# Optimization experiments

Hardware: AMD Instinct MI355X
Metric: run time of the kernel (lower is better)

The kernel has to match this reference:

```python
import jax, jax.numpy as jnp
import numpy as np

B, D, E, H, L = 32768, 512, 10, 128, 2  # batch, input_dim, max_charts, expert hidden, latent_dim
RH1, RH2 = 256, 128                      # router hidden sizes
TAU = 3.0


def setup_inputs() -> dict:
    key = jax.random.key(0)
    ks = jax.random.split(key, 16)
    rnd = lambda k, *s: (jax.random.normal(k, s, jnp.float32) * 0.05)
    return {
        "x": jax.random.normal(ks[0], (B, D), jnp.float32),
        "u": jax.random.uniform(ks[1], (B, E), jnp.float32),
        # router params (last layer init ~ N(0, 0.01), bias 0, as in _init_router)
        "rw1": rnd(ks[2], D, RH1), "rb1": jnp.zeros((RH1,), jnp.float32),
        "rw2": rnd(ks[3], RH1, RH2), "rb2": jnp.zeros((RH2,), jnp.float32),
        "rw3": jax.random.normal(ks[4], (RH2, E), jnp.float32) * 0.01,
        "rb3": jnp.zeros((E,), jnp.float32),
        # stacked expert params: all 10 experts batched along leading dim
        "ew1": rnd(ks[5], E, D, H), "eb1": rnd(ks[6], E, H),
        "ew2": rnd(ks[7], E, H, H), "eb2": rnd(ks[8], E, H),
        "ew3": rnd(ks[9], E, H, L), "eb3": rnd(ks[10], E, L),
    }


def reference(x, u, rw1, rb1, rw2, rb2, rw3, rb3, ew1, eb1, ew2, eb2, ew3, eb3):
    # router MLP: D -> 256 -> 128 -> E
    h = jax.nn.relu(x @ rw1 + rb1)
    h = jax.nn.relu(h @ rw2 + rb2)
    logits = h @ rw3 + rb3                                  # [B, E]
    # gumbel_softmax(tau=3.0, hard=False): softmax((logits + gumbel)/tau)
    g = -jnp.log(-jnp.log(jnp.clip(u, 1e-10, 1.0)) + 1e-10)
    weights = jax.nn.softmax((logits + g) / TAU, axis=1)    # [B, E]
    # all 10 experts as batched GEMMs (fuses the python loop over charts)
    h1 = jax.nn.relu(jnp.einsum('bi,eio->beo', x, ew1) + eb1[None])   # [B, E, H]
    h2 = jax.nn.relu(jnp.einsum('beh,eho->beo', h1, ew2) + eb2[None]) # [B, E, H]
    zc = jnp.einsum('beh,ehl->bel', h2, ew3) + eb3[None]              # [B, E, L]
    z = jnp.einsum('be,bel->bl', weights, zc)                         # [B, L]
    chart_outputs = jnp.transpose(zc, (1, 0, 2))                      # [E, B, L]
    return z, weights, chart_outputs
```

## Files before the change

kernel.cpp:

```cpp
#include <hip/hip_runtime.h>
#include <stdint.h>

typedef __bf16 bf16x8 __attribute__((ext_vector_type(8)));
typedef float floatx4 __attribute__((ext_vector_type(4)));
typedef unsigned short ushort_t;

__device__ __forceinline__ ushort_t bf16rne(float f) {
    union { float f; unsigned u; } v; v.f = f;
    return (ushort_t)((v.u + 0x7fffu + ((v.u >> 16) & 1u)) >> 16);
}

__device__ __forceinline__ void gl_lds16(const ushort_t* g, ushort_t* l) {
    __builtin_amdgcn_global_load_lds(
        (const __attribute__((address_space(1))) unsigned int*)g,
        (__attribute__((address_space(3))) unsigned int*)l, 16, 0, 0);
}


__global__ void prep(const float* __restrict__ x, ushort_t* __restrict__ x16,
                     const float* __restrict__ ew1, ushort_t* __restrict__ ew1t,
                     const float* __restrict__ ew2, ushort_t* __restrict__ ew2t,
                     const float* __restrict__ rw1, ushort_t* __restrict__ rw1t,
                     const float* __restrict__ rw2, ushort_t* __restrict__ rw2t) {
    __shared__ ushort_t sT[64 * 65];
    int b = blockIdx.x, tid = threadIdx.x;
    if (b < 16384) {
        int i = b * 256 + tid;
        float4 f = ((const float4*)x)[i];
        union { ushort_t s[4]; uint2 v; } pk;
        pk.s[0] = bf16rne(f.x); pk.s[1] = bf16rne(f.y);
        pk.s[2] = bf16rne(f.z); pk.s[3] = bf16rne(f.w);
        ((uint2*)x16)[i] = pk.v;
        return;
    }
    const float* in; ushort_t* outp; int K, N, k0, n0;
    int i = b - 16384;
    if (i < 160) {
        int e = i >> 4, t = i & 15;
        in = ew1 + e * 65536; outp = ew1t + e * 65536;
        K = 512; N = 128; k0 = (t >> 1) * 64; n0 = (t & 1) * 64;
    } else if (i < 200) {
        i -= 160; int e = i >> 2, t = i & 3;
        in = ew2 + e * 16384; outp = ew2t + e * 16384;
        K = 128; N = 128; k0 = (t >> 1) * 64; n0 = (t & 1) * 64;
    } else if (i < 232) {
        i -= 200; in = rw1; outp = rw1t;
        K = 512; N = 256; k0 = (i >> 2) * 64; n0 = (i & 3) * 64;
    } else {
        i -= 232; in = rw2; outp = rw2t;
        K = 256; N = 128; k0 = (i >> 1) * 64; n0 = (i & 1) * 64;
    }
    {
        int c = tid & 63, r0 = tid >> 6;
#pragma unroll
        for (int p = 0; p < 16; ++p) {
            int r = r0 * 16 + p;
            sT[c * 65 + r] = bf16rne(in[(size_t)(k0 + r) * N + n0 + c]);
        }
        __syncthreads();
        int rr = tid & 63, c0 = tid >> 6;
#pragma unroll
        for (int p = 0; p < 16; ++p) {
            int cc = c0 * 16 + p;
            outp[(size_t)(n0 + cc) * K + k0 + rr] = sT[cc * 65 + rr];
        }
    }
}

__global__ __launch_bounds__(256, 3)
void fused_main(const ushort_t* __restrict__ x16,
                const ushort_t* __restrict__ rw1t, const float* __restrict__ rb1,
                const ushort_t* __restrict__ rw2t, const float* __restrict__ rb2,
                const float* __restrict__ rw3, const float* __restrict__ rb3,
                const float* __restrict__ u,
                const ushort_t* __restrict__ ew1t, const ushort_t* __restrict__ ew2t,
                const float* __restrict__ eb1, const float* __restrict__ eb2,
                const float* __restrict__ ew3, const float* __restrict__ eb3,
                float* __restrict__ wts, float* __restrict__ chart) {
    __shared__ alignas(16) ushort_t sXW[8192];
    __shared__ alignas(16) ushort_t sH1[16384];
    __shared__ float sB1[128];
    __shared__ float sB2[128];
    __shared__ float sW3e[256];
    __shared__ float zbuf[128][2];

    const int tid = threadIdx.x;
    const int id = blockIdx.x;
    const int wave = tid >> 6, lane = tid & 63;
    const int ln15 = lane & 15, q = lane >> 4;
    const int wm = (wave & 1) * 64, wn = (wave >> 1) * 64;
    const int mhalf = wm >> 6, nhalf = wn >> 6;
    const int rl = lane >> 2, cl = lane & 3;
    const int sw = (cl ^ ((rl >> 1) & 3)) * 8;
    const int rg0 = wave * 2, rg1 = rg0 + 1;
    const int fslot = (4 * ln15 + (q ^ ((ln15 >> 1) & 3))) * 8;

    if (id < 256) {
        const int rb = (id & 7) * 32 + (id >> 3);
        if (tid < 128) sB2[tid] = rb2[tid];
        const ushort_t* xblk = x16 + (size_t)rb * 128 * 512;

        floatx4 acc2[4][4];
#pragma unroll
        for (int i = 0; i < 4; ++i)
#pragma unroll
            for (int j = 0; j < 4; ++j) acc2[i][j] = (floatx4){0.f, 0.f, 0.f, 0.f};

        for (int ph = 0; ph < 2; ++ph) {
            if (tid < 128) sB1[tid] = rb1[ph * 128 + tid];
            const ushort_t* w1base = rw1t + (size_t)ph * 128 * 512;

            floatx4 acc[4][4];
#pragma unroll
            for (int i = 0; i < 4; ++i)
#pragma unroll
                for (int j = 0; j < 4; ++j) acc[i][j] = (floatx4){0.f, 0.f, 0.f, 0.f};

            for (int k0 = 0; k0 < 512; k0 += 32) {
                __syncthreads();
                gl_lds16(xblk + (size_t)(rg0 * 16 + rl) * 512 + k0 + sw, &sXW[rg0 * 512]);
                gl_lds16(xblk + (size_t)(rg1 * 16 + rl) * 512 + k0 + sw, &sXW[rg1 * 512]);
                gl_lds16(w1base + (size_t)(rg0 * 16 + rl) * 512 + k0 + sw, &sXW[4096 + rg0 * 512]);
                gl_lds16(w1base + (size_t)(rg1 * 16 + rl) * 512 + k0 + sw, &sXW[4096 + rg1 * 512]);
                __syncthreads();
                bf16x8 a[4], b[4];
#pragma unroll
                for (int t = 0; t < 4; ++t) a[t] = *(const bf16x8*)(&sXW[4096 + (mhalf * 4 + t) * 512 + fslot]);
#pragma unroll
                for (int t = 0; t < 4; ++t) b[t] = *(const bf16x8*)(&sXW[(nhalf * 4 + t) * 512 + fslot]);
#pragma unroll
                for (int i = 0; i < 4; ++i)
#pragma unroll
                    for (int j = 0; j < 4; ++j)
                        acc[i][j] = __builtin_amdgcn_mfma_f32_16x16x32_bf16(a[i], b[j], acc[i][j], 0, 0, 0);
            }

#pragma unroll
            for (int i = 0; i < 4; ++i) {
                int hbase = wm + 16 * i;
                int kh = hbase >> 5;
                int qhi = (hbase >> 4) & 1;
                int slotq = 2 * qhi + (q >> 1);
                int h0 = hbase + q * 4;
#pragma unroll
                for (int j = 0; j < 4; ++j) {
                    union { ushort_t s[4]; uint2 v; } pk;
#pragma unroll
                    for (int r = 0; r < 4; ++r)
                        pk.s[r] = bf16rne(fmaxf(acc[i][j][r] + sB1[h0 + r], 0.f));
                    *(uint2*)(&sH1[kh * 4096 + (nhalf * 4 + j) * 512 + slotq * 128 + ln15 * 8 + (q & 1) * 4]) = pk.v;
                }
            }

            for (int p = 0; p < 2; ++p) {
                __syncthreads();
#pragma unroll
                for (int r = 0; r < 4; ++r) {
                    int s = wave * 4 + r;
                    int khl = s >> 3, rg = s & 7;
                    int kh = p * 2 + khl;
                    gl_lds16(rw2t + (size_t)(rg * 16 + rl) * 256 + ph * 128 + kh * 32 + sw, &sXW[s * 512]);
                }
                __syncthreads();
#pragma unroll
                for (int khl = 0; khl < 2; ++khl) {
                    int kh = p * 2 + khl;
                    bf16x8 a[4], b[4];
#pragma unroll
                    for (int t = 0; t < 4; ++t) a[t] = *(const bf16x8*)(&sXW[(khl * 8 + mhalf * 4 + t) * 512 + fslot]);
#pragma unroll
                    for (int t = 0; t < 4; ++t) b[t] = *(const bf16x8*)(&sH1[kh * 4096 + (nhalf * 4 + t) * 512 + lane * 8]);
#pragma unroll
                    for (int i = 0; i < 4; ++i)
#pragma unroll
                        for (int j = 0; j < 4; ++j)
                            acc2[i][j] = __builtin_amdgcn_mfma_f32_16x16x32_bf16(a[i], b[j], acc2[i][j], 0, 0, 0);
                }
            }
        }

        __syncthreads();
        float* sw3r = (float*)sXW;
        float* lgbuf = (float*)(&sXW[2560]);
        for (int i = tid; i < 1280; i += 256) sw3r[i] = rw3[i];
        __syncthreads();

        float lg[4][10];
#pragma unroll
        for (int j = 0; j < 4; ++j)
#pragma unroll
            for (int ee = 0; ee < 10; ++ee) lg[j][ee] = 0.f;
#pragma unroll
        for (int i = 0; i < 4; ++i) {
#pragma unroll
            for (int r = 0; r < 4; ++r) {
                int n = wm + i * 16 + q * 4 + r;
                float bias = sB2[n];
                const float* w3r = &sw3r[n * 10];
#pragma unroll
                for (int j = 0; j < 4; ++j) {
                    float val = fmaxf(acc2[i][j][r] + bias, 0.f);
#pragma unroll
                    for (int ee = 0; ee < 10; ++ee) lg[j][ee] += val * w3r[ee];
                }
            }
        }
#pragma unroll
        for (int j = 0; j < 4; ++j)
#pragma unroll
            for (int ee = 0; ee < 10; ++ee) {
                lg[j][ee] += __shfl_xor(lg[j][ee], 16, 64);
                lg[j][ee] += __shfl_xor(lg[j][ee], 32, 64);
            }
        if (wm == 0 && q == 0) {
#pragma unroll
            for (int j = 0; j < 4; ++j) {
                int row = wn + 16 * j + ln15;
#pragma unroll
                for (int ee = 0; ee < 10; ++ee) lgbuf[row * 10 + ee] = lg[j][ee];
            }
        }
        __syncthreads();
        if (wm == 64 && q == 0) {
#pragma unroll
            for (int j = 0; j < 4; ++j) {
                int row = wn + 16 * j + ln15;
#pragma unroll
                for (int ee = 0; ee < 10; ++ee) lgbuf[row * 10 + ee] += lg[j][ee];
            }
        }
        __syncthreads();
        if (tid < 128) {
            int grow = rb * 128 + tid;
            float v[10], mx = -1e30f;
#pragma unroll
            for (int ee = 0; ee < 10; ++ee) {
                float uu = u[(size_t)grow * 10 + ee];
                uu = fminf(fmaxf(uu, 1e-10f), 1.0f);
                float g = -logf(-logf(uu) + 1e-10f);
                v[ee] = (lgbuf[tid * 10 + ee] + rb3[ee] + g) * (1.0f / 3.0f);
                mx = fmaxf(mx, v[ee]);
            }
            float s = 0.f;
#pragma unroll
            for (int ee = 0; ee < 10; ++ee) { v[ee] = expf(v[ee] - mx); s += v[ee]; }
            float inv = 1.0f / s;
#pragma unroll
            for (int ee = 0; ee < 10; ++ee) wts[(size_t)grow * 10 + ee] = v[ee] * inv;
        }
    } else {
        const int eid = id - 256;
        const int xcd = eid & 7, local = eid >> 3;
        const int e = local % 10;
        const int rb = xcd * 32 + local / 10;

        if (tid < 128) sB1[tid] = eb1[e * 128 + tid];
        else sB2[tid - 128] = eb2[e * 128 + (tid - 128)];
        sW3e[tid] = ew3[e * 256 + tid];

        const ushort_t* xblk = x16 + (size_t)rb * 128 * 512;
        const ushort_t* w1 = ew1t + (size_t)e * 128 * 512;
        const ushort_t* w2 = ew2t + (size_t)e * 128 * 128;

        {
            floatx4 acc[4][4];
#pragma unroll
            for (int i = 0; i < 4; ++i)
#pragma unroll
                for (int j = 0; j < 4; ++j) acc[i][j] = (floatx4){0.f, 0.f, 0.f, 0.f};

            for (int k0 = 0; k0 < 512; k0 += 32) {
                __syncthreads();
                gl_lds16(xblk + (size_t)(rg0 * 16 + rl) * 512 + k0 + sw, &sXW[rg0 * 512]);
                gl_lds16(xblk + (size_t)(rg1 * 16 + rl) * 512 + k0 + sw, &sXW[rg1 * 512]);
                gl_lds16(w1 + (size_t)(rg0 * 16 + rl) * 512 + k0 + sw, &sXW[4096 + rg0 * 512]);
                gl_lds16(w1 + (size_t)(rg1 * 16 + rl) * 512 + k0 + sw, &sXW[4096 + rg1 * 512]);
                __syncthreads();
                bf16x8 a[4], b[4];
#pragma unroll
                for (int t = 0; t < 4; ++t) a[t] = *(const bf16x8*)(&sXW[4096 + (mhalf * 4 + t) * 512 + fslot]);
#pragma unroll
                for (int t = 0; t < 4; ++t) b[t] = *(const bf16x8*)(&sXW[(nhalf * 4 + t) * 512 + fslot]);
#pragma unroll
                for (int i = 0; i < 4; ++i)
#pragma unroll
                    for (int j = 0; j < 4; ++j)
                        acc[i][j] = __builtin_amdgcn_mfma_f32_16x16x32_bf16(a[i], b[j], acc[i][j], 0, 0, 0);
            }

#pragma unroll
            for (int i = 0; i < 4; ++i) {
                int hbase = wm + 16 * i;
                int kh = hbase >> 5;
                int qhi = (hbase >> 4) & 1;
                int slotq = 2 * qhi + (q >> 1);
                int h0 = hbase + q * 4;
#pragma unroll
                for (int j = 0; j < 4; ++j) {
                    union { ushort_t s[4]; uint2 v; } pk;
#pragma unroll
                    for (int r = 0; r < 4; ++r)
                        pk.s[r] = bf16rne(fmaxf(acc[i][j][r] + sB1[h0 + r], 0.f));
                    *(uint2*)(&sH1[kh * 4096 + (nhalf * 4 + j) * 512 + slotq * 128 + ln15 * 8 + (q & 1) * 4]) = pk.v;
                }
            }
        }

        floatx4 acc2[4][4];
#pragma unroll
        for (int i = 0; i < 4; ++i)
#pragma unroll
            for (int j = 0; j < 4; ++j) acc2[i][j] = (floatx4){0.f, 0.f, 0.f, 0.f};

        for (int p = 0; p < 2; ++p) {
            __syncthreads();
#pragma unroll
            for (int r = 0; r < 4; ++r) {
                int s = wave * 4 + r;
                int khl = s >> 3, rg = s & 7;
                int kh = p * 2 + khl;
                gl_lds16(w2 + (size_t)(rg * 16 + rl) * 128 + kh * 32 + sw, &sXW[s * 512]);
            }
            __syncthreads();
#pragma unroll
            for (int khl = 0; khl < 2; ++khl) {
                int kh = p * 2 + khl;
                bf16x8 a[4], b[4];
#pragma unroll
                for (int t = 0; t < 4; ++t) a[t] = *(const bf16x8*)(&sXW[(khl * 8 + mhalf * 4 + t) * 512 + fslot]);
#pragma unroll
                for (int t = 0; t < 4; ++t) b[t] = *(const bf16x8*)(&sH1[kh * 4096 + (nhalf * 4 + t) * 512 + lane * 8]);
#pragma unroll
                for (int i = 0; i < 4; ++i)
#pragma unroll
                    for (int j = 0; j < 4; ++j)
                        acc2[i][j] = __builtin_amdgcn_mfma_f32_16x16x32_bf16(a[i], b[j], acc2[i][j], 0, 0, 0);
            }
        }

        float zc0[4] = {0.f, 0.f, 0.f, 0.f}, zc1[4] = {0.f, 0.f, 0.f, 0.f};
#pragma unroll
        for (int i = 0; i < 4; ++i) {
            int o0 = wm + i * 16 + q * 4;
#pragma unroll
            for (int r = 0; r < 4; ++r) {
                int o = o0 + r;
                float w3a = sW3e[2 * o], w3b = sW3e[2 * o + 1];
                float bias = sB2[o];
#pragma unroll
                for (int j = 0; j < 4; ++j) {
                    float val = fmaxf(acc2[i][j][r] + bias, 0.f);
                    zc0[j] += val * w3a;
                    zc1[j] += val * w3b;
                }
            }
        }
#pragma unroll
        for (int j = 0; j < 4; ++j) {
            zc0[j] += __shfl_xor(zc0[j], 16, 64);
            zc0[j] += __shfl_xor(zc0[j], 32, 64);
            zc1[j] += __shfl_xor(zc1[j], 16, 64);
            zc1[j] += __shfl_xor(zc1[j], 32, 64);
        }
        if (wm == 0 && q == 0) {
#pragma unroll
            for (int j = 0; j < 4; ++j) {
                int row = wn + j * 16 + ln15;
                zbuf[row][0] = zc0[j];
                zbuf[row][1] = zc1[j];
            }
        }
        __syncthreads();
        if (wm == 64 && q == 0) {
#pragma unroll
            for (int j = 0; j < 4; ++j) {
                int row = wn + j * 16 + ln15;
                zbuf[row][0] += zc0[j];
                zbuf[row][1] += zc1[j];
            }
        }
        __syncthreads();
        {
            int row = tid >> 1, l = tid & 1;
            int grow = rb * 128 + row;
            chart[(size_t)e * 65536 + (size_t)grow * 2 + l] = zbuf[row][l] + eb3[e * 2 + l];
        }
    }
}

__global__ void z_final(const float* __restrict__ w, const float* __restrict__ chart,
                        float* __restrict__ z) {
    int row = blockIdx.x * 256 + threadIdx.x;
    float z0 = 0.f, z1 = 0.f;
#pragma unroll
    for (int e = 0; e < 10; ++e) {
        float we = w[(size_t)row * 10 + e];
        float2 c = *(const float2*)(&chart[(size_t)e * 65536 + (size_t)row * 2]);
        z0 += we * c.x;
        z1 += we * c.y;
    }
    float2 o; o.x = z0; o.y = z1;
    *(float2*)(&z[(size_t)row * 2]) = o;
}

extern "C" void kernel_launch(void* const* d_in, const int* in_sizes, int n_in,
                              void* d_out, int out_size, void* d_ws, size_t ws_size,
                              hipStream_t stream) {
    const float* x = (const float*)d_in[0];
    const float* u = (const float*)d_in[1];
    const float* rw1 = (const float*)d_in[2];
    const float* rb1 = (const float*)d_in[3];
    const float* rw2 = (const float*)d_in[4];
    const float* rb2 = (const float*)d_in[5];
    const float* rw3 = (const float*)d_in[6];
    const float* rb3 = (const float*)d_in[7];
    const float* ew1 = (const float*)d_in[8];
    const float* eb1 = (const float*)d_in[9];
    const float* ew2 = (const float*)d_in[10];
    const float* eb2 = (const float*)d_in[11];
    const float* ew3 = (const float*)d_in[12];
    const float* eb3 = (const float*)d_in[13];
    float* out = (float*)d_out;
    float* z = out;
    float* wts = out + 65536;
    float* chart = out + 393216;

    ushort_t* x16  = (ushort_t*)d_ws;
    ushort_t* ew1t = x16 + 16777216;
    ushort_t* ew2t = ew1t + 655360;
    ushort_t* rw1t = ew2t + 163840;
    ushort_t* rw2t = rw1t + 131072;

    prep<<<16624, 256, 0, stream>>>(x, x16, ew1, ew1t, ew2, ew2t, rw1, rw1t, rw2, rw2t);

    fused_main<<<2816, 256, 0, stream>>>(x16, rw1t, rb1, rw2t, rb2, rw3, rb3, u,
                                         ew1t, ew2t, eb1, eb2, ew3, eb3,
                                         wts, chart);

    z_final<<<128, 256, 0, stream>>>(wts, chart, z);
}
```

Measured before the change: 220.9 us.

## Process two experts per block to share x tile loads in first GEMM

```diff
diff --git a/kernel.cpp b/kernel.cpp
--- a/kernel.cpp
+++ b/kernel.cpp
@@ -67,7 +67,7 @@
     }
 }
 
-__global__ __launch_bounds__(256, 3)
+__global__ __launch_bounds__(256, 2)
 void fused_main(const ushort_t* __restrict__ x16,
                 const ushort_t* __restrict__ rw1t, const float* __restrict__ rb1,
                 const ushort_t* __restrict__ rw2t, const float* __restrict__ rb2,
@@ -77,11 +77,11 @@
                 const float* __restrict__ eb1, const float* __restrict__ eb2,
                 const float* __restrict__ ew3, const float* __restrict__ eb3,
                 float* __restrict__ wts, float* __restrict__ chart) {
-    __shared__ alignas(16) ushort_t sXW[8192];
+    __shared__ alignas(16) ushort_t sXW[16384];
     __shared__ alignas(16) ushort_t sH1[16384];
-    __shared__ float sB1[128];
-    __shared__ float sB2[128];
-    __shared__ float sW3e[256];
+    __shared__ float sB1[2][128];
+    __shared__ float sB2[2][128];
+    __shared__ float sW3e[2][256];
     __shared__ float zbuf[128][2];
 
     const int tid = threadIdx.x;
@@ -97,7 +97,8 @@
 
     if (id < 256) {
         const int rb = (id & 7) * 32 + (id >> 3);
-        if (tid < 128) sB2[tid] = rb2[tid];
+        if (tid < 128) sB2[0][tid] = rb2[tid];
+        else sB2[1][tid - 128] = rb2[tid];
         const ushort_t* xblk = x16 + (size_t)rb * 128 * 512;
 
         floatx4 acc2[4][4];
@@ -107,7 +108,7 @@
             for (int j = 0; j < 4; ++j) acc2[i][j] = (floatx4){0.f, 0.f, 0.f, 0.f};
 
         for (int ph = 0; ph < 2; ++ph) {
-            if (tid < 128) sB1[tid] = rb1[ph * 128 + tid];
+            if (tid < 128) sB1[0][tid] = rb1[ph * 128 + tid];
             const ushort_t* w1base = rw1t + (size_t)ph * 128 * 512;
 
             floatx4 acc[4][4];
@@ -147,7 +148,7 @@
                     union { ushort_t s[4]; uint2 v; } pk;
 #pragma unroll
                     for (int r = 0; r < 4; ++r)
-                        pk.s[r] = bf16rne(fmaxf(acc[i][j][r] + sB1[h0 + r], 0.f));
+                        pk.s[r] = bf16rne(fmaxf(acc[i][j][r] + sB1[0][h0 + r], 0.f));
                     *(uint2*)(&sH1[kh * 4096 + (nhalf * 4 + j) * 512 + slotq * 128 + ln15 * 8 + (q & 1) * 4]) = pk.v;
                 }
             }
@@ -195,7 +196,7 @@
 #pragma unroll
             for (int r = 0; r < 4; ++r) {
                 int n = wm + i * 16 + q * 4 + r;
-                float bias = sB2[n];
+                float bias = n < 128 ? sB2[0][n] : sB2[1][n - 128];
                 const float* w3r = &sw3r[n * 10];
 #pragma unroll
                 for (int j = 0; j < 4; ++j) {
@@ -251,42 +252,62 @@
     } else {
         const int eid = id - 256;
         const int xcd = eid & 7, local = eid >> 3;
-        const int e = local % 10;
-        const int rb = xcd * 32 + local / 10;
-
-        if (tid < 128) sB1[tid] = eb1[e * 128 + tid];
-        else sB2[tid - 128] = eb2[e * 128 + (tid - 128)];
-        sW3e[tid] = ew3[e * 256 + tid];
+        const int pr = local % 5;
+        const int rb = xcd * 32 + local / 5;
+        const int e0 = pr * 2;
+
+        if (tid < 128) {
+            sB1[0][tid] = eb1[e0 * 128 + tid];
+            sB2[0][tid] = eb2[e0 * 128 + tid];
+        } else {
+            sB1[1][tid - 128] = eb1[(e0 + 1) * 128 + (tid - 128)];
+            sB2[1][tid - 128] = eb2[(e0 + 1) * 128 + (tid - 128)];
+        }
+        sW3e[0][tid] = ew3[e0 * 256 + tid];
+        sW3e[1][tid] = ew3[(e0 + 1) * 256 + tid];
 
         const ushort_t* xblk = x16 + (size_t)rb * 128 * 512;
-        const ushort_t* w1 = ew1t + (size_t)e * 128 * 512;
-        const ushort_t* w2 = ew2t + (size_t)e * 128 * 128;
-
-        {
-            floatx4 acc[4][4];
+        const ushort_t* w1a = ew1t + (size_t)e0 * 65536;
+        const ushort_t* w1b = w1a + 65536;
+
+        floatx4 accA[4][4], accB[4][4];
+#pragma unroll
+        for (int i = 0; i < 4; ++i)
+#pragma unroll
+            for (int j = 0; j < 4; ++j) {
+                accA[i][j] = (floatx4){0.f, 0.f, 0.f, 0.f};
+                accB[i][j] = (floatx4){0.f, 0.f, 0.f, 0.f};
+            }
+
+        for (int k0 = 0; k0 < 512; k0 += 32) {
+            __syncthreads();
+            gl_lds16(xblk + (size_t)(rg0 * 16 + rl) * 512 + k0 + sw, &sXW[rg0 * 512]);
+            gl_lds16(xblk + (size_t)(rg1 * 16 + rl) * 512 + k0 + sw, &sXW[rg1 * 512]);
+            gl_lds16(w1a + (size_t)(rg0 * 16 + rl) * 512 + k0 + sw, &sXW[4096 + rg0 * 512]);
+            gl_lds16(w1a + (size_t)(rg1 * 16 + rl) * 512 + k0 + sw, &sXW[4096 + rg1 * 512]);
+            gl_lds16(w1b + (size_t)(rg0 * 16 + rl) * 512 + k0 + sw, &sXW[8192 + rg0 * 512]);
+            gl_lds16(w1b + (size_t)(rg1 * 16 + rl) * 512 + k0 + sw, &sXW[8192 + rg1 * 512]);
+            __syncthreads();
+            bf16x8 a0[4], a1[4], b[4];
+#pragma unroll
+            for (int t = 0; t < 4; ++t) b[t] = *(const bf16x8*)(&sXW[(nhalf * 4 + t) * 512 + fslot]);
+#pragma unroll
+            for (int t = 0; t < 4; ++t) a0[t] = *(const bf16x8*)(&sXW[4096 + (mhalf * 4 + t) * 512 + fslot]);
+#pragma unroll
+            for (int t = 0; t < 4; ++t) a1[t] = *(const bf16x8*)(&sXW[8192 + (mhalf * 4 + t) * 512 + fslot]);
 #pragma unroll
             for (int i = 0; i < 4; ++i)
 #pragma unroll
-                for (int j = 0; j < 4; ++j) acc[i][j] = (floatx4){0.f, 0.f, 0.f, 0.f};
-
-            for (int k0 = 0; k0 < 512; k0 += 32) {
-                __syncthreads();
-                gl_lds16(xblk + (size_t)(rg0 * 16 + rl) * 512 + k0 + sw, &sXW[rg0 * 512]);
-                gl_lds16(xblk + (size_t)(rg1 * 16 + rl) * 512 + k0 + sw, &sXW[rg1 * 512]);
-                gl_lds16(w1 + (size_t)(rg0 * 16 + rl) * 512 + k0 + sw, &sXW[4096 + rg0 * 512]);
-                gl_lds16(w1 + (size_t)(rg1 * 16 + rl) * 512 + k0 + sw, &sXW[4096 + rg1 * 512]);
-                __syncthreads();
-                bf16x8 a[4], b[4];
-#pragma unroll
-                for (int t = 0; t < 4; ++t) a[t] = *(const bf16x8*)(&sXW[4096 + (mhalf * 4 + t) * 512 + fslot]);
-#pragma unroll
-                for (int t = 0; t < 4; ++t) b[t] = *(const bf16x8*)(&sXW[(nhalf * 4 + t) * 512 + fslot]);
-#pragma unroll
-                for (int i = 0; i < 4; ++i)
-#pragma unroll
-                    for (int j = 0; j < 4; ++j)
-                        acc[i][j] = __builtin_amdgcn_mfma_f32_16x16x32_bf16(a[i], b[j], acc[i][j], 0, 0, 0);
-            }
+                for (int j = 0; j < 4; ++j) {
+                    accA[i][j] = __builtin_amdgcn_mfma_f32_16x16x32_bf16(a0[i], b[j], accA[i][j], 0, 0, 0);
+                    accB[i][j] = __builtin_amdgcn_mfma_f32_16x16x32_bf16(a1[i], b[j], accB[i][j], 0, 0, 0);
+                }
+        }
+
+#pragma unroll
+        for (int ex = 0; ex < 2; ++ex) {
+            const int e = e0 + ex;
+            const ushort_t* w2 = ew2t + (size_t)e * 16384;
 
 #pragma unroll
             for (int i = 0; i < 4; ++i) {
@@ -299,91 +320,93 @@
                 for (int j = 0; j < 4; ++j) {
                     union { ushort_t s[4]; uint2 v; } pk;
 #pragma unroll
-                    for (int r = 0; r < 4; ++r)
-                        pk.s[r] = bf16rne(fmaxf(acc[i][j][r] + sB1[h0 + r], 0.f));
+                    for (int r = 0; r < 4; ++r) {
+                        float av = ex == 0 ? accA[i][j][r] : accB[i][j][r];
+                        pk.s[r] = bf16rne(fmaxf(av + sB1[ex][h0 + r], 0.f));
+                    }
                     *(uint2*)(&sH1[kh * 4096 + (nhalf * 4 + j) * 512 + slotq * 128 + ln15 * 8 + (q & 1) * 4]) = pk.v;
                 }
             }
-        }
-
-        floatx4 acc2[4][4];
-#pragma unroll
-        for (int i = 0; i < 4; ++i)
-#pragma unroll
-            for (int j = 0; j < 4; ++j) acc2[i][j] = (floatx4){0.f, 0.f, 0.f, 0.f};
-
-        for (int p = 0; p < 2; ++p) {
+
+            floatx4 acc2[4][4];
+#pragma unroll
+            for (int i = 0; i < 4; ++i)
+#pragma unroll
+                for (int j = 0; j < 4; ++j) acc2[i][j] = (floatx4){0.f, 0.f, 0.f, 0.f};
+
+            for (int p = 0; p < 2; ++p) {
+                __syncthreads();
+#pragma unroll
+                for (int r = 0; r < 4; ++r) {
+                    int s = wave * 4 + r;
+                    int khl = s >> 3, rg = s & 7;
+                    int kh = p * 2 + khl;
+                    gl_lds16(w2 + (size_t)(rg * 16 + rl) * 128 + kh * 32 + sw, &sXW[s * 512]);
+                }
+                __syncthreads();
+#pragma unroll
+                for (int khl = 0; khl < 2; ++khl) {
+                    int kh = p * 2 + khl;
+                    bf16x8 a[4], b[4];
+#pragma unroll
+                    for (int t = 0; t < 4; ++t) a[t] = *(const bf16x8*)(&sXW[(khl * 8 + mhalf * 4 + t) * 512 + fslot]);
+#pragma unroll
+                    for (int t = 0; t < 4; ++t) b[t] = *(const bf16x8*)(&sH1[kh * 4096 + (nhalf * 4 + t) * 512 + lane * 8]);
+#pragma unroll
+                    for (int i = 0; i < 4; ++i)
+#pragma unroll
+                        for (int j = 0; j < 4; ++j)
+                            acc2[i][j] = __builtin_amdgcn_mfma_f32_16x16x32_bf16(a[i], b[j], acc2[i][j], 0, 0, 0);
+                }
+            }
+
+            float zc0[4] = {0.f, 0.f, 0.f, 0.f}, zc1[4] = {0.f, 0.f, 0.f, 0.f};
+#pragma unroll
+            for (int i = 0; i < 4; ++i) {
+                int o0 = wm + i * 16 + q * 4;
+#pragma unroll
+                for (int r = 0; r < 4; ++r) {
+                    int o = o0 + r;
+                    float w3a = sW3e[ex][2 * o], w3b = sW3e[ex][2 * o + 1];
+                    float bias = sB2[ex][o];
+#pragma unroll
+                    for (int j = 0; j < 4; ++j) {
+                        float val = fmaxf(acc2[i][j][r] + bias, 0.f);
+                        zc0[j] += val * w3a;
+                        zc1[j] += val * w3b;
+                    }
+                }
+            }
+#pragma unroll
+            for (int j = 0; j < 4; ++j) {
+                zc0[j] += __shfl_xor(zc0[j], 16, 64);
+                zc0[j] += __shfl_xor(zc0[j], 32, 64);
+                zc1[j] += __shfl_xor(zc1[j], 16, 64);
+                zc1[j] += __shfl_xor(zc1[j], 32, 64);
+            }
+            if (wm == 0 && q == 0) {
+#pragma unroll
+                for (int j = 0; j < 4; ++j) {
+                    int row = wn + j * 16 + ln15;
+                    zbuf[row][0] = zc0[j];
+                    zbuf[row][1] = zc1[j];
+                }
+            }
             __syncthreads();
-#pragma unroll
-            for (int r = 0; r < 4; ++r) {
-                int s = wave * 4 + r;
-                int khl = s >> 3, rg = s & 7;
-                int kh = p * 2 + khl;
-                gl_lds16(w2 + (size_t)(rg * 16 + rl) * 128 + kh * 32 + sw, &sXW[s * 512]);
+            if (wm == 64 && q == 0) {
+#pragma unroll
+                for (int j = 0; j < 4; ++j) {
+                    int row = wn + j * 16 + ln15;
+                    zbuf[row][0] += zc0[j];
+                    zbuf[row][1] += zc1[j];
+                }
             }
             __syncthreads();
-#pragma unroll
-            for (int khl = 0; khl < 2; ++khl) {
-                int kh = p * 2 + khl;
-                bf16x8 a[4], b[4];
-#pragma unroll
-                for (int t = 0; t < 4; ++t) a[t] = *(const bf16x8*)(&sXW[(khl * 8 + mhalf * 4 + t) * 512 + fslot]);
-#pragma unroll
-                for (int t = 0; t < 4; ++t) b[t] = *(const bf16x8*)(&sH1[kh * 4096 + (nhalf * 4 + t) * 512 + lane * 8]);
-#pragma unroll
-                for (int i = 0; i < 4; ++i)
-#pragma unroll
-                    for (int j = 0; j < 4; ++j)
-                        acc2[i][j] = __builtin_amdgcn_mfma_f32_16x16x32_bf16(a[i], b[j], acc2[i][j], 0, 0, 0);
-            }
-        }
-
-        float zc0[4] = {0.f, 0.f, 0.f, 0.f}, zc1[4] = {0.f, 0.f, 0.f, 0.f};
-#pragma unroll
-        for (int i = 0; i < 4; ++i) {
-            int o0 = wm + i * 16 + q * 4;
-#pragma unroll
-            for (int r = 0; r < 4; ++r) {
-                int o = o0 + r;
-                float w3a = sW3e[2 * o], w3b = sW3e[2 * o + 1];
-                float bias = sB2[o];
-#pragma unroll
-                for (int j = 0; j < 4; ++j) {
-                    float val = fmaxf(acc2[i][j][r] + bias, 0.f);
-                    zc0[j] += val * w3a;
-                    zc1[j] += val * w3b;
-                }
-            }
-        }
-#pragma unroll
-        for (int j = 0; j < 4; ++j) {
-            zc0[j] += __shfl_xor(zc0[j], 16, 64);
-            zc0[j] += __shfl_xor(zc0[j], 32, 64);
-            zc1[j] += __shfl_xor(zc1[j], 16, 64);
-            zc1[j] += __shfl_xor(zc1[j], 32, 64);
-        }
-        if (wm == 0 && q == 0) {
-#pragma unroll
-            for (int j = 0; j < 4; ++j) {
-                int row = wn + j * 16 + ln15;
-                zbuf[row][0] = zc0[j];
-                zbuf[row][1] = zc1[j];
-            }
-        }
-        __syncthreads();
-        if (wm == 64 && q == 0) {
-#pragma unroll
-            for (int j = 0; j < 4; ++j) {
-                int row = wn + j * 16 + ln15;
-                zbuf[row][0] += zc0[j];
-                zbuf[row][1] += zc1[j];
-            }
-        }
-        __syncthreads();
-        {
-            int row = tid >> 1, l = tid & 1;
-            int grow = rb * 128 + row;
-            chart[(size_t)e * 65536 + (size_t)grow * 2 + l] = zbuf[row][l] + eb3[e * 2 + l];
+            {
+                int row = tid >> 1, l = tid & 1;
+                int grow = rb * 128 + row;
+                chart[(size_t)e * 65536 + (size_t)grow * 2 + l] = zbuf[row][l] + eb3[e * 2 + l];
+            }
         }
     }
 }
@@ -433,7 +456,7 @@
 
     prep<<<16624, 256, 0, stream>>>(x, x16, ew1, ew1t, ew2, ew2t, rw1, rw1t, rw2, rw2t);
 
-    fused_main<<<2816, 256, 0, stream>>>(x16, rw1t, rb1, rw2t, rb2, rw3, rb3, u,
+    fused_main<<<1536, 256, 0, stream>>>(x16, rw1t, rb1, rw2t, rb2, rw3, rb3, u,
                                          ew1t, ew2t, eb1, eb2, ew3, eb3,
                                          wts, chart);
 
```

Measured after the change: 217.8 us. Within noise of the previous version (-1.4%).
